# Performance work log

Measured on AMD Instinct MI355X. Metric: run time of the kernel, lower is better.

Reference implementation:

```python
import jax, jax.numpy as jnp
import numpy as np

B, S, D = 4, 2048, 1024

def setup_inputs() -> dict:
    key = jax.random.key(0)
    kv, kk, kq, kw = jax.random.split(key, 4)
    scale = 1.0 / np.sqrt(D)
    v = jax.random.normal(kv, (B, S, D), dtype=jnp.float32)
    k = jax.random.normal(kk, (B, S, D), dtype=jnp.float32)
    q = jax.random.normal(kq, (B, S, D), dtype=jnp.float32)
    wi = jax.random.normal(kw, (D, D), dtype=jnp.float32) * scale
    mask = jnp.tril(jnp.ones((S, S), dtype=bool))[None, :, :]  # causal [1,S,S]
    return {"v": v, "k": k, "q": q, "wi": wi, "mask": mask}

def reference(v, k, q, wi, mask):
    # project q, k, v with the shared weight wi
    q = q @ wi
    k = k @ wi
    v = v @ wi
    # scaled dot-product scores [B,S,S]
    scores = jnp.einsum('bqd,bkd->bqk', q, k) / jnp.sqrt(jnp.asarray(q.shape[-1], q.dtype))
    scores = jnp.where(mask, scores, jnp.asarray(-1e10, scores.dtype))
    attn = jax.nn.softmax(scores, axis=-1)
    # residual: q + attn @ v
    return q + jnp.einsum('bqk,bkd->bqd', attn, v)
```

## Files before the change

kernel.cpp:

```cpp
#include <hip/hip_runtime.h>
#include <hip/hip_bf16.h>

typedef __hip_bfloat16 bf16;
typedef short bf16x8 __attribute__((ext_vector_type(8)));
typedef float f32x4 __attribute__((ext_vector_type(4)));

#define HT 16384

__device__ __forceinline__ void gload16(const void* g, void* l) {
    __builtin_amdgcn_global_load_lds(
        (const __attribute__((address_space(1))) void*)g,
        (__attribute__((address_space(3))) void*)l, 16, 0, 0);
}

__device__ __forceinline__ void stage_half(char* lds, const bf16* src, int ld,
                                           int rowbase, int k0, int slotIdx,
                                           int tid)
{
    char* dst = lds + (size_t)slotIdx * HT + tid * 16;
    const int sub = tid >> 3;
    const int cb  = ((tid & 7) ^ (sub & 7)) << 4;
    #pragma unroll
    for (int p = 0; p < 2; ++p) {
        const int row = p * 64 + sub;
        const char* g = (const char*)(src + (size_t)(rowbase + row) * ld + k0) + cb;
        gload16(g, dst + p * 8192);
    }
}

__device__ __forceinline__ void stage_q(char* lds, const bf16* src, int ld,
                                        int rowbase, int k0, int slotIdx,
                                        int tid)
{
    char* dst = lds + (size_t)slotIdx * HT + tid * 16;
    #pragma unroll
    for (int p = 0; p < 4; ++p) {
        const int s = p * 256 + tid;
        const int row = s >> 3;
        const int cb = ((s & 7) ^ (row & 7)) << 4;
        const char* g = (const char*)(src + (size_t)(rowbase + row) * ld + k0) + cb;
        gload16(g, dst + p * 4096);
    }
}

__device__ __forceinline__ bf16x8 ldsfrag(const char* lds, int slotIdx,
                                          int row, int ks, int cb0)
{
    return *(const bf16x8*)(lds + (size_t)slotIdx * HT
                            + row * 128 + (cb0 ^ (ks << 6)));
}

__device__ __forceinline__ float bf2f(short s) {
    union { float f; unsigned u; } c;
    c.u = ((unsigned)(unsigned short)s) << 16;
    return c.f;
}

#define GEMM256_BODY(A_, lda_, B_, ldb_, brow_, bcol_)                        \
    f32x4 acc[4][4] = {};                                                     \
    bf16x8 af[4][2], bv[4][2];                                                \
    stage_half(lds, A_, lda_, brow_,       0, 0, tid);                        \
    stage_half(lds, A_, lda_, brow_ + 128, 0, 1, tid);                        \
    stage_half(lds, B_, ldb_, bcol_,       0, 6, tid);                        \
    stage_half(lds, A_, lda_, brow_,      64, 2, tid);                        \
    stage_half(lds, A_, lda_, brow_ + 128,64, 3, tid);                        \
    stage_half(lds, B_, ldb_, bcol_,     64, 7, tid);                         \
    asm volatile("s_waitcnt vmcnt(6)" ::: "memory");                          \
    __builtin_amdgcn_s_barrier();                                             \
    for (int t = 0; t < 16; ++t) {                                            \
        const int aslot = (t % 3) * 2 + hA;                                   \
        const int bslot = 6 + (t & 1);                                        \
        const int a2    = ((t + 2) % 3) * 2;                                  \
        const int k2    = min(t + 2, 15) << 6;                                \
        _Pragma("unroll") for (int m = 0; m < 4; ++m)                         \
        _Pragma("unroll") for (int ks = 0; ks < 2; ++ks)                      \
            af[m][ks] = ldsfrag(lds, aslot, rA + m * 16 + fr, ks, cb0);       \
        _Pragma("unroll") for (int n = 0; n < 4; ++n)                         \
        _Pragma("unroll") for (int ks = 0; ks < 2; ++ks)                      \
            bv[n][ks] = ldsfrag(lds, bslot, rB + n * 16 + fr, ks, cb0);       \
        stage_half(lds, A_, lda_, brow_,       k2, a2,     tid);              \
        stage_half(lds, A_, lda_, brow_ + 128, k2, a2 + 1, tid);              \
        __builtin_amdgcn_s_barrier();                                         \
        __builtin_amdgcn_s_setprio(1);                                        \
        MF8(0)                                                                \
        __builtin_amdgcn_s_setprio(0);                                        \
        __builtin_amdgcn_s_barrier();                                         \
        stage_half(lds, B_, ldb_, bcol_, k2, bslot, tid);                     \
        __builtin_amdgcn_s_barrier();                                         \
        __builtin_amdgcn_s_setprio(1);                                        \
        MF8(2)                                                                \
        __builtin_amdgcn_s_setprio(0);                                        \
        asm volatile("s_waitcnt vmcnt(6)" ::: "memory");                      \
        __builtin_amdgcn_s_barrier();                                         \
    }

#define MF8(n0)                                                               \
    _Pragma("unroll") for (int m = 0; m < 4; ++m)                             \
    _Pragma("unroll") for (int dn = 0; dn < 2; ++dn)                          \
    _Pragma("unroll") for (int ks = 0; ks < 2; ++ks)                          \
        acc[m][(n0)+dn] = __builtin_amdgcn_mfma_f32_16x16x32_bf16(            \
            af[m][ks], bv[(n0)+dn][ks], acc[m][(n0)+dn], 0, 0, 0);

template<int MODE>
__launch_bounds__(512, 2)
__global__ void gemm_a256(const bf16* __restrict__ A, const bf16* __restrict__ B,
                          bf16* __restrict__ Cb, float* __restrict__ Cf)
{
    extern __shared__ char lds[];
    const int gx = gridDim.x;
    const int nwg = gx * gridDim.y;
    const int chunk = nwg >> 3;
    const int orig = blockIdx.y * gx + blockIdx.x;
    const int wk2 = (orig & 7) * chunk + (orig >> 3);
    const int bi = wk2 / gx, bj = wk2 % gx;
    const int brow = bi * 256, bcol = bj * 128;

    const int tid  = threadIdx.x;
    const int lane = tid & 63;
    const int w    = tid >> 6;
    const int wm   = w >> 1, wn = w & 1;
    const int fr   = lane & 15, fq = lane >> 4;
    const int cb0  = ((fr & 7) ^ fq) << 4;
    const int hA   = wm >> 1;
    const int rA   = (wm & 1) * 64;
    const int rB   = wn * 64;

    GEMM256_BODY(A, 1024, B, 1024, brow, bcol)

    #pragma unroll
    for (int mf = 0; mf < 4; ++mf) {
        const int r0 = brow + wm * 64 + mf * 16 + fq * 4;
        #pragma unroll
        for (int nf = 0; nf < 4; ++nf) {
            const int c = bcol + wn * 64 + nf * 16 + fr;
            #pragma unroll
            for (int j = 0; j < 4; ++j) {
                if (MODE == 0)
                    Cb[(size_t)(r0 + j) * 1024 + c] =
                        __float2bfloat16(acc[mf][nf][j]);
                else
                    Cf[(size_t)(r0 + j) * 1024 + c] = acc[mf][nf][j];
            }
        }
    }
}

__launch_bounds__(512, 2)
__global__ void scores256(const bf16* __restrict__ qG, const bf16* __restrict__ kb,
                          bf16* __restrict__ P)
{
    extern __shared__ char lds[];
    const int orig = blockIdx.y * 8 + blockIdx.x;
    const int wk2 = (orig & 7) * 36 + (orig >> 3);
    const int bz = wk2 / 72;
    const int j  = wk2 % 72;
    int bi = 0;
    #pragma unroll
    for (int i = 1; i < 8; ++i) if (i * (i + 1) <= j) bi = i;
    const int bj = j - bi * (bi + 1);
    const int brow = bi * 256, bcol = bj * 128;

    const bf16* A = qG + (size_t)bz * 2048 * 1024;
    const bf16* B = kb + (size_t)bz * 2048 * 1024;
    bf16* Cp = P + (size_t)bz * 2048 * 2048;

    const int tid  = threadIdx.x;
    const int lane = tid & 63;
    const int w    = tid >> 6;
    const int wm   = w >> 1, wn = w & 1;
    const int fr   = lane & 15, fq = lane >> 4;
    const int cb0  = ((fr & 7) ^ fq) << 4;
    const int hA   = wm >> 1;
    const int rA   = (wm & 1) * 64;
    const int rB   = wn * 64;

    GEMM256_BODY(A, 1024, B, 1024, brow, bcol)

    #pragma unroll
    for (int mf = 0; mf < 4; ++mf) {
        const int r0 = brow + wm * 64 + mf * 16 + fq * 4;
        #pragma unroll
        for (int nf = 0; nf < 4; ++nf) {
            const int c = bcol + wn * 64 + nf * 16 + fr;
            #pragma unroll
            for (int j2 = 0; j2 < 4; ++j2)
                Cp[(size_t)(r0 + j2) * 2048 + c] =
                    __float2bfloat16(acc[mf][nf][j2] * 0.03125f);
        }
    }
}

__device__ __forceinline__ void tile128pv(char* lds, const bf16* A, const bf16* B,
                                          bf16* Cb, const bf16* Res,
                                          int lda, int ldb, int ldcb,
                                          int brow, int bcol, int NT, int tid)
{
    const int lane = tid & 63;
    const int w    = tid >> 6;
    const int wm   = w >> 1, wn = w & 1;
    const int fr   = lane & 15, fq = lane >> 4;
    const int cb0  = ((fr & 7) ^ fq) << 4;

    f32x4 acc[4][4] = {};
    bf16x8 af[4][2], bv[4][2];

    stage_q(lds, A, lda, brow, 0,  0, tid);
    stage_q(lds, B, ldb, bcol, 0,  3, tid);
    stage_q(lds, A, lda, brow, 64, 1, tid);
    stage_q(lds, B, ldb, bcol, 64, 4, tid);
    asm volatile("s_waitcnt vmcnt(8)" ::: "memory");
    __builtin_amdgcn_s_barrier();

    for (int t = 0; t < NT; ++t) {
        const int aslot = t % 3, bslot = 3 + (t & 1);
        const int k2 = min(t + 2, NT - 1) << 6;

        #pragma unroll
        for (int m = 0; m < 4; ++m)
            #pragma unroll
            for (int ks = 0; ks < 2; ++ks)
                af[m][ks] = ldsfrag(lds, aslot, wm * 64 + m * 16 + fr, ks, cb0);
        #pragma unroll
        for (int n = 0; n < 4; ++n)
            #pragma unroll
            for (int ks = 0; ks < 2; ++ks)
                bv[n][ks] = ldsfrag(lds, bslot, wn * 64 + n * 16 + fr, ks, cb0);
        stage_q(lds, A, lda, brow, k2, (t + 2) % 3, tid);
        __builtin_amdgcn_s_barrier();
        __builtin_amdgcn_s_setprio(1);
        #pragma unroll
        for (int m = 0; m < 4; ++m)
            #pragma unroll
            for (int n = 0; n < 2; ++n)
                #pragma unroll
                for (int ks = 0; ks < 2; ++ks)
                    acc[m][n] = __builtin_amdgcn_mfma_f32_16x16x32_bf16(
                        af[m][ks], bv[n][ks], acc[m][n], 0, 0, 0);
        __builtin_amdgcn_s_setprio(0);
        __builtin_amdgcn_s_barrier();

        stage_q(lds, B, ldb, bcol, k2, bslot, tid);
        __builtin_amdgcn_s_barrier();
        __builtin_amdgcn_s_setprio(1);
        #pragma unroll
        for (int m = 0; m < 4; ++m)
            #pragma unroll
            for (int n = 2; n < 4; ++n)
                #pragma unroll
                for (int ks = 0; ks < 2; ++ks)
                    acc[m][n] = __builtin_amdgcn_mfma_f32_16x16x32_bf16(
                        af[m][ks], bv[n][ks], acc[m][n], 0, 0, 0);
        __builtin_amdgcn_s_setprio(0);
        asm volatile("s_waitcnt vmcnt(8)" ::: "memory");
        __builtin_amdgcn_s_barrier();
    }

    #pragma unroll
    for (int mf = 0; mf < 4; ++mf) {
        const int r0 = brow + wm * 64 + mf * 16 + fq * 4;
        #pragma unroll
        for (int nf = 0; nf < 4; ++nf) {
            const int c = bcol + wn * 64 + nf * 16 + fr;
            #pragma unroll
            for (int j = 0; j < 4; ++j)
                Cb[(size_t)(r0 + j) * ldcb + c] = __float2bfloat16(
                    acc[mf][nf][j] +
                    __bfloat162float(Res[(size_t)(r0 + j) * ldcb + c]));
        }
    }
}

__launch_bounds__(256, 2)
__global__ void pv128(const bf16* __restrict__ P, const bf16* __restrict__ vT,
                      const bf16* __restrict__ qb, bf16* __restrict__ Y)
{
    extern __shared__ char lds[];
    const int x    = blockIdx.x;
    const int bs   = x & 7;
    const int half = (x >> 3) & 1;
    const int bz   = (x >> 4) & 3;
    const int bj   = x >> 6;
    const int bi   = half ? (15 - bs) : bs;

    tile128pv(lds,
              P + (size_t)bz * 2048 * 2048,
              vT + (size_t)bz * 1024 * 2048,
              Y + (size_t)bz * 2048 * 1024,
              qb + (size_t)bz * 2048 * 1024,
              2048, 2048, 1024,
              bi * 128, bj * 128, 2 * (bi + 1), threadIdx.x);
}

__global__ void convert_qk_w(const float* __restrict__ q, const float* __restrict__ k,
                             const float* __restrict__ wi,
                             bf16* __restrict__ qb, bf16* __restrict__ kb,
                             bf16* __restrict__ Wb)
{
    const int N8 = 8192 * 1024 / 8;
    const int W8 = 1024 * 1024 / 8;
    const int total = 2 * N8 + W8;
    for (int i = blockIdx.x * 256 + threadIdx.x; i < total; i += gridDim.x * 256) {
        const float4* s;
        bf16* dst;
        int j;
        if (i < N8)            { s = (const float4*)q;  dst = qb; j = i; }
        else if (i < 2 * N8)   { s = (const float4*)k;  dst = kb; j = i - N8; }
        else                   { s = (const float4*)wi; dst = Wb; j = i - 2 * N8; }
        float4 a = s[2 * j], b = s[2 * j + 1];
        float vals[8] = {a.x, a.y, a.z, a.w, b.x, b.y, b.z, b.w};
        union { short h[8]; bf16x8 v8; } o;
        #pragma unroll
        for (int e = 0; e < 8; ++e) {
            bf16 hh = __float2bfloat16(vals[e]);
            o.h[e] = *(short*)&hh;
        }
        ((bf16x8*)dst)[j] = o.v8;
    }
}

__global__ void transpose_vwi(const float* __restrict__ v,
                              const float* __restrict__ wi,
                              bf16* __restrict__ vT, bf16* __restrict__ Wt)
{
    __shared__ float t[32][33];
    const int z = blockIdx.z;
    const int lx = threadIdx.x & 31, ly = threadIdx.x >> 5;
    if (z < 4) {
        const int d0 = blockIdx.x * 32, s0 = blockIdx.y * 32;
        const float* src = v + (size_t)z * 2048 * 1024;
        bf16* dst = vT + (size_t)z * 1024 * 2048;
        for (int i = ly; i < 32; i += 8)
            t[i][lx] = src[(size_t)(s0 + i) * 1024 + d0 + lx];
        __syncthreads();
        for (int i = ly; i < 32; i += 8)
            dst[(size_t)(d0 + i) * 2048 + s0 + lx] = __float2bfloat16(t[lx][i]);
    } else {
        if (blockIdx.y >= 32) return;
        const int n0 = blockIdx.x * 32, k0 = blockIdx.y * 32;
        for (int i = ly; i < 32; i += 8)
            t[i][lx] = wi[(size_t)(k0 + i) * 1024 + n0 + lx];
        __syncthreads();
        for (int i = ly; i < 32; i += 8)
            Wt[(size_t)(n0 + i) * 1024 + k0 + lx] = __float2bfloat16(t[lx][i]);
    }
}

__launch_bounds__(256)
__global__ void softmax_rows(bf16* __restrict__ P)
{
    const int wid = threadIdx.x >> 6, lane = threadIdx.x & 63;
    const int r = blockIdx.x * 4 + wid, b = blockIdx.y;
    bf16* row = P + ((size_t)b * 2048 + r) * 2048;
    const int nv  = r + 1;
    const int rup = (r & ~127) + 128;

    float vals[4][8];
    float m = -1e30f;
    #pragma unroll
    for (int c = 0; c < 4; ++c) {
        const int k0 = c * 512 + lane * 8;
        if (k0 < rup) {
            bf16x8 x = *(const bf16x8*)(row + k0);
            #pragma unroll
            for (int j = 0; j < 8; ++j) {
                float f = (k0 + j < nv) ? bf2f(x[j]) : -1e30f;
                vals[c][j] = f;
                m = fmaxf(m, f);
            }
        } else {
            #pragma unroll
            for (int j = 0; j < 8; ++j) vals[c][j] = -1e30f;
        }
    }
    #pragma unroll
    for (int o = 32; o; o >>= 1) m = fmaxf(m, __shfl_xor(m, o));

    float sum = 0.f;
    #pragma unroll
    for (int c = 0; c < 4; ++c)
        #pragma unroll
        for (int j = 0; j < 8; ++j) {
            float e = __expf(vals[c][j] - m);
            vals[c][j] = e;
            sum += e;
        }
    #pragma unroll
    for (int o = 32; o; o >>= 1) sum += __shfl_xor(sum, o);
    const float inv = 1.0f / sum;

    #pragma unroll
    for (int c = 0; c < 4; ++c) {
        const int k0 = c * 512 + lane * 8;
        if (k0 < rup) {
            union { short h[8]; bf16x8 v8; } o;
            #pragma unroll
            for (int j = 0; j < 8; ++j) {
                bf16 hh = __float2bfloat16(vals[c][j] * inv);
                o.h[j] = *(short*)&hh;
            }
            *(bf16x8*)(row + k0) = o.v8;
        }
    }
}

extern "C" void kernel_launch(void* const* d_in, const int* in_sizes, int n_in,
                              void* d_out, int out_size, void* d_ws, size_t ws_size,
                              hipStream_t stream)
{
    const float* v  = (const float*)d_in[0];
    const float* k  = (const float*)d_in[1];
    const float* q  = (const float*)d_in[2];
    const float* wi = (const float*)d_in[3];
    float* out = (float*)d_out;

    char* ws = (char*)d_ws;
    const size_t MB = 1u << 20;
    bf16* Wb = (bf16*)(ws);
    bf16* Wt = (bf16*)(ws + 2 * MB);
    bf16* G  = (bf16*)(ws + 4 * MB);
    bf16* qb = (bf16*)(ws + 6 * MB);
    bf16* kb = (bf16*)(ws + 22 * MB);
    bf16* vT = (bf16*)(ws + 38 * MB);
    bf16* qG = (bf16*)(ws + 54 * MB);
    bf16* Y  = (bf16*)(ws + 70 * MB);
    bf16* P  = (bf16*)(ws + 86 * MB);

    (void)hipFuncSetAttribute((const void*)gemm_a256<0>,
            hipFuncAttributeMaxDynamicSharedMemorySize, 131072);
    (void)hipFuncSetAttribute((const void*)gemm_a256<2>,
            hipFuncAttributeMaxDynamicSharedMemorySize, 131072);
    (void)hipFuncSetAttribute((const void*)scores256,
            hipFuncAttributeMaxDynamicSharedMemorySize, 131072);
    (void)hipFuncSetAttribute((const void*)pv128,
            hipFuncAttributeMaxDynamicSharedMemorySize, 81920);

    convert_qk_w<<<2048, 256, 0, stream>>>(q, k, wi, qb, kb, Wb);
    transpose_vwi<<<dim3(32, 64, 5), 256, 0, stream>>>(v, wi, vT, Wt);

    gemm_a256<0><<<dim3(8, 4), 512, 131072, stream>>>(Wb, Wb, G, nullptr);

    gemm_a256<0><<<dim3(8, 32), 512, 131072, stream>>>(qb, G, qG, nullptr);

    scores256<<<dim3(8, 36), 512, 131072, stream>>>(qG, kb, P);

    softmax_rows<<<dim3(512, 4), 256, 0, stream>>>(P);

    pv128<<<dim3(512), 256, 81920, stream>>>(P, vT, qb, Y);

    gemm_a256<2><<<dim3(8, 32), 512, 131072, stream>>>(Y, Wt, nullptr, out);
}
```

Before: 176.4 us.

## Use 256x256 tiles with 8-phase pipeline for causal scores GEMM

Replaces the 256x128 scores kernel with a 256x256 tile kernel. Eight waves each compute a 128x64 block, and the A/B loads are split into four staged phases that interleave global-to-LDS loads with MFMA groups. The grid is halved to 144 lower-triangular tiles, and the kernel uses 160KB LDS with one block per CU, trading occupancy for higher arithmetic intensity per tile. The pv128 block-index mapping is also reordered so that bj and bz vary before the half selector.

```diff
diff --git a/kernel.cpp b/kernel.cpp
--- a/kernel.cpp
+++ b/kernel.cpp
@@ -55,6 +55,13 @@
     c.u = ((unsigned)(unsigned short)s) << 16;
     return c.f;
 }
+
+#define MF8(n0)                                                               \
+    _Pragma("unroll") for (int m = 0; m < 4; ++m)                             \
+    _Pragma("unroll") for (int dn = 0; dn < 2; ++dn)                          \
+    _Pragma("unroll") for (int ks = 0; ks < 2; ++ks)                          \
+        acc[m][(n0)+dn] = __builtin_amdgcn_mfma_f32_16x16x32_bf16(            \
+            af[m][ks], bv[(n0)+dn][ks], acc[m][(n0)+dn], 0, 0, 0);
 
 #define GEMM256_BODY(A_, lda_, B_, ldb_, brow_, bcol_)                        \
     f32x4 acc[4][4] = {};                                                     \
@@ -94,13 +101,6 @@
         __builtin_amdgcn_s_barrier();                                         \
     }
 
-#define MF8(n0)                                                               \
-    _Pragma("unroll") for (int m = 0; m < 4; ++m)                             \
-    _Pragma("unroll") for (int dn = 0; dn < 2; ++dn)                          \
-    _Pragma("unroll") for (int ks = 0; ks < 2; ++ks)                          \
-        acc[m][(n0)+dn] = __builtin_amdgcn_mfma_f32_16x16x32_bf16(            \
-            af[m][ks], bv[(n0)+dn][ks], acc[m][(n0)+dn], 0, 0, 0);
-
 template<int MODE>
 __launch_bounds__(512, 2)
 __global__ void gemm_a256(const bf16* __restrict__ A, const bf16* __restrict__ B,
@@ -145,21 +145,20 @@
     }
 }
 
-__launch_bounds__(512, 2)
-__global__ void scores256(const bf16* __restrict__ qG, const bf16* __restrict__ kb,
-                          bf16* __restrict__ P)
+__launch_bounds__(512, 1)
+__global__ void scores8(const bf16* __restrict__ qG, const bf16* __restrict__ kb,
+                        bf16* __restrict__ P)
 {
     extern __shared__ char lds[];
     const int orig = blockIdx.y * 8 + blockIdx.x;
-    const int wk2 = (orig & 7) * 36 + (orig >> 3);
-    const int bz = wk2 / 72;
-    const int j  = wk2 % 72;
-    int bi = 0;
-    #pragma unroll
-    for (int i = 1; i < 8; ++i) if (i * (i + 1) <= j) bi = i;
-    const int bj = j - bi * (bi + 1);
-    const int brow = bi * 256, bcol = bj * 128;
-
+    const int wk2 = (orig & 7) * 18 + (orig >> 3);
+    const int bz = wk2 / 36;
+    const int j  = wk2 % 36;
+    int bi = (int)((__fsqrt_rn(8.0f * j + 1.0f) - 1.0f) * 0.5f);
+    while ((bi + 1) * (bi + 2) / 2 <= j) ++bi;
+    while (bi * (bi + 1) / 2 > j) --bi;
+    const int bj = j - bi * (bi + 1) / 2;
+    const int brow = bi * 256, bcol = bj * 256;
     const bf16* A = qG + (size_t)bz * 2048 * 1024;
     const bf16* B = kb + (size_t)bz * 2048 * 1024;
     bf16* Cp = P + (size_t)bz * 2048 * 2048;
@@ -167,25 +166,105 @@
     const int tid  = threadIdx.x;
     const int lane = tid & 63;
     const int w    = tid >> 6;
-    const int wm   = w >> 1, wn = w & 1;
+    const int wm   = w >> 2;
+    const int wn   = w & 3;
+    const int bh   = wn >> 1;
+    const int rBl  = (wn & 1) * 64;
     const int fr   = lane & 15, fq = lane >> 4;
     const int cb0  = ((fr & 7) ^ fq) << 4;
-    const int hA   = wm >> 1;
-    const int rA   = (wm & 1) * 64;
-    const int rB   = wn * 64;
-
-    GEMM256_BODY(A, 1024, B, 1024, brow, bcol)
-
-    #pragma unroll
-    for (int mf = 0; mf < 4; ++mf) {
-        const int r0 = brow + wm * 64 + mf * 16 + fq * 4;
+
+    f32x4 acc[8][4] = {};
+    bf16x8 af0[4][2], af1[4][2], bv0[2][2], bv1[2][2];
+
+#define AS(t,h) ((((t) % 3) * 2) + (h))
+#define BS(t,h) (6 + (((t) & 1) * 2) + (h))
+
+    stage_half(lds, A, 1024, brow,       0, AS(0,0), tid);
+    stage_half(lds, A, 1024, brow + 128, 0, AS(0,1), tid);
+    stage_half(lds, B, 1024, bcol,       0, BS(0,0), tid);
+    stage_half(lds, B, 1024, bcol + 128, 0, BS(0,1), tid);
+    stage_half(lds, A, 1024, brow,      64, AS(1,0), tid);
+    stage_half(lds, A, 1024, brow + 128,64, AS(1,1), tid);
+    stage_half(lds, B, 1024, bcol,     64, BS(1,0), tid);
+    asm volatile("s_waitcnt vmcnt(6)" ::: "memory");
+    __builtin_amdgcn_s_barrier();
+
+#define MFQ(MH, NH, AF, BV)                                                   \
+    _Pragma("unroll") for (int m = 0; m < 4; ++m)                             \
+    _Pragma("unroll") for (int n = 0; n < 2; ++n)                             \
+    _Pragma("unroll") for (int ks = 0; ks < 2; ++ks)                          \
+        acc[(MH)*4+m][(NH)*2+n] = __builtin_amdgcn_mfma_f32_16x16x32_bf16(    \
+            AF[m][ks], BV[n][ks], acc[(MH)*4+m][(NH)*2+n], 0, 0, 0);
+
+    for (int t = 0; t < 16; ++t) {
+        const int kN  = min(t + 1, 15) << 6;
+        const int kNN = min(t + 2, 15) << 6;
+        const int as  = AS(t, wm);
+        const int bs2 = BS(t, bh);
+
+        #pragma unroll
+        for (int m = 0; m < 4; ++m)
+            #pragma unroll
+            for (int ks = 0; ks < 2; ++ks)
+                af0[m][ks] = ldsfrag(lds, as, m * 16 + fr, ks, cb0);
+        #pragma unroll
+        for (int n = 0; n < 2; ++n)
+            #pragma unroll
+            for (int ks = 0; ks < 2; ++ks)
+                bv0[n][ks] = ldsfrag(lds, bs2, rBl + n * 16 + fr, ks, cb0);
+        stage_half(lds, B, 1024, bcol + 128, kN, BS(t + 1, 1), tid);
+        __builtin_amdgcn_s_barrier();
+        __builtin_amdgcn_s_setprio(1);
+        MFQ(0, 0, af0, bv0)
+        __builtin_amdgcn_s_setprio(0);
+        __builtin_amdgcn_s_barrier();
+
+        #pragma unroll
+        for (int m = 0; m < 4; ++m)
+            #pragma unroll
+            for (int ks = 0; ks < 2; ++ks)
+                af1[m][ks] = ldsfrag(lds, as, 64 + m * 16 + fr, ks, cb0);
+        stage_half(lds, A, 1024, brow, kNN, AS(t + 2, 0), tid);
+        __builtin_amdgcn_s_barrier();
+        __builtin_amdgcn_s_setprio(1);
+        MFQ(1, 0, af1, bv0)
+        __builtin_amdgcn_s_setprio(0);
+        __builtin_amdgcn_s_barrier();
+
+        #pragma unroll
+        for (int n = 0; n < 2; ++n)
+            #pragma unroll
+            for (int ks = 0; ks < 2; ++ks)
+                bv1[n][ks] = ldsfrag(lds, bs2, rBl + 32 + n * 16 + fr, ks, cb0);
+        stage_half(lds, A, 1024, brow + 128, kNN, AS(t + 2, 1), tid);
+        __builtin_amdgcn_s_barrier();
+        __builtin_amdgcn_s_setprio(1);
+        MFQ(1, 1, af1, bv1)
+        __builtin_amdgcn_s_setprio(0);
+        __builtin_amdgcn_s_barrier();
+
+        stage_half(lds, B, 1024, bcol, kNN, BS(t + 2, 0), tid);
+        __builtin_amdgcn_s_barrier();
+        __builtin_amdgcn_s_setprio(1);
+        MFQ(0, 1, af0, bv1)
+        __builtin_amdgcn_s_setprio(0);
+        asm volatile("s_waitcnt vmcnt(6)" ::: "memory");
+        __builtin_amdgcn_s_barrier();
+    }
+#undef MFQ
+#undef AS
+#undef BS
+
+    #pragma unroll
+    for (int mf = 0; mf < 8; ++mf) {
+        const int r0 = brow + wm * 128 + mf * 16 + fq * 4;
         #pragma unroll
         for (int nf = 0; nf < 4; ++nf) {
             const int c = bcol + wn * 64 + nf * 16 + fr;
             #pragma unroll
-            for (int j2 = 0; j2 < 4; ++j2)
-                Cp[(size_t)(r0 + j2) * 2048 + c] =
-                    __float2bfloat16(acc[mf][nf][j2] * 0.03125f);
+            for (int jj = 0; jj < 4; ++jj)
+                Cp[(size_t)(r0 + jj) * 2048 + c] =
+                    __float2bfloat16(acc[mf][nf][jj] * 0.03125f);
         }
     }
 }
@@ -275,12 +354,12 @@
                       const bf16* __restrict__ qb, bf16* __restrict__ Y)
 {
     extern __shared__ char lds[];
-    const int x    = blockIdx.x;
-    const int bs   = x & 7;
-    const int half = (x >> 3) & 1;
-    const int bz   = (x >> 4) & 3;
-    const int bj   = x >> 6;
-    const int bi   = half ? (15 - bs) : bs;
+    const int x  = blockIdx.x;
+    const int u  = x & 255;
+    const int bs = u & 7;
+    const int bj = (u >> 3) & 7;
+    const int bz = u >> 6;
+    const int bi = (x >> 8) ? (15 - bs) : bs;
 
     tile128pv(lds,
               P + (size_t)bz * 2048 * 2048,
@@ -429,8 +508,8 @@
             hipFuncAttributeMaxDynamicSharedMemorySize, 131072);
     (void)hipFuncSetAttribute((const void*)gemm_a256<2>,
             hipFuncAttributeMaxDynamicSharedMemorySize, 131072);
-    (void)hipFuncSetAttribute((const void*)scores256,
-            hipFuncAttributeMaxDynamicSharedMemorySize, 131072);
+    (void)hipFuncSetAttribute((const void*)scores8,
+            hipFuncAttributeMaxDynamicSharedMemorySize, 163840);
     (void)hipFuncSetAttribute((const void*)pv128,
             hipFuncAttributeMaxDynamicSharedMemorySize, 81920);
 
@@ -441,7 +520,7 @@
 
     gemm_a256<0><<<dim3(8, 32), 512, 131072, stream>>>(qb, G, qG, nullptr);
 
-    scores256<<<dim3(8, 36), 512, 131072, stream>>>(qG, kb, P);
+    scores8<<<dim3(8, 18), 512, 163840, stream>>>(qG, kb, P);
 
     softmax_rows<<<dim3(512, 4), 256, 0, stream>>>(P);
 
```

Result: faster. 164.9 us (-6.5%).
